# Optimization experiments

Measured on AMD Instinct MI355X. Metric: run time of the kernel, lower is better.

The kernel has to match this reference:

```python
import jax, jax.numpy as jnp
import numpy as np

T = 512   # timesteps (also used as batch-index count for packing)
B = 512   # batch (must equal T for this module's packing to be consistent)
D = 300   # state_dim
H = 128   # hidden_state_dim
E = 64    # embedding_dim
EGO = 12  # ego_state slice fed to the LSTMCell


def setup_inputs() -> dict:
    key = jax.random.key(0)
    ks = jax.random.split(key, 10)
    k = float(1.0 / np.sqrt(H))  # torch LSTMCell uniform init bound
    state = jax.random.normal(ks[0], (T, B, D), dtype=jnp.float32)
    hidden_state = jax.random.normal(ks[1], (B, H), dtype=jnp.float32) * 0.1
    cell_state = jax.random.normal(ks[2], (B, H), dtype=jnp.float32) * 0.1
    len_sequence = jax.random.randint(ks[3], (T,), 1, T + 1, dtype=jnp.int64 if jax.config.jax_enable_x64 else jnp.int32)
    W_ih = jax.random.uniform(ks[4], (4 * H, EGO), minval=-k, maxval=k, dtype=jnp.float32)
    W_hh = jax.random.uniform(ks[5], (4 * H, H), minval=-k, maxval=k, dtype=jnp.float32)
    b_ih = jax.random.uniform(ks[6], (4 * H,), minval=-k, maxval=k, dtype=jnp.float32)
    b_hh = jax.random.uniform(ks[7], (4 * H,), minval=-k, maxval=k, dtype=jnp.float32)
    W_emb = jax.random.normal(ks[8], (E, D + H), dtype=jnp.float32) * 0.05
    b_emb = jnp.zeros((E,), dtype=jnp.float32)
    return dict(state=state, hidden_state=hidden_state, cell_state=cell_state,
                len_sequence=len_sequence, W_ih=W_ih, W_hh=W_hh, b_ih=b_ih,
                b_hh=b_hh, W_emb=W_emb, b_emb=b_emb)


def _pack_indices(L):
    # tmp_output[t][:L[t]] concat over t -> flat indices into [T*B, .] (row-major t,b)
    idx_rnn = np.concatenate([t * B + np.arange(int(L[t])) for t in range(T)]) if T else np.zeros((0,), np.int32)
    # state.permute(1,0,2)[b][:L[b]] concat over b -> flat indices into [B*T, .] (row-major b,t)
    idx_state = np.concatenate([b * T + np.arange(int(L[b])) for b in range(B)]) if B else np.zeros((0,), np.int32)
    return jnp.asarray(idx_rnn, jnp.int32), jnp.asarray(idx_state, jnp.int32)


def _lstm_scan(x_seq, h0, c0, W_ih, W_hh, b_ih, b_hh):
    # torch.nn.LSTMCell math; gate order [i, f, g, o]
    def step(carry, x_t):
        h, c = carry
        gates = x_t @ W_ih.T + b_ih + h @ W_hh.T + b_hh  # [B, 4H]
        i, f, g, o = jnp.split(gates, 4, axis=-1)
        c_new = jax.nn.sigmoid(f) * c + jax.nn.sigmoid(i) * jnp.tanh(g)
        h_new = jax.nn.sigmoid(o) * jnp.tanh(c_new)
        return (h_new, c_new), h_new
    _, hs = jax.lax.scan(step, (h0, c0), x_seq)
    return hs  # [T, B, H]


def reference(state, hidden_state, cell_state, len_sequence, W_ih, W_hh, b_ih, b_hh, W_emb, b_emb):
    L = np.asarray(len_sequence)
    idx_rnn, idx_state = _pack_indices(L)
    rnn_input = state[:, :, :EGO]                               # [T, B, 12]
    hs = _lstm_scan(rnn_input, hidden_state, cell_state, W_ih, W_hh, b_ih, b_hh)  # [T, B, H]
    rnn_packed = hs.reshape(T * B, H)[idx_rnn]                  # [N, H]
    state_packed = jnp.transpose(state, (1, 0, 2)).reshape(B * T, D)[idx_state]  # [N, D]
    feats = jnp.concatenate([state_packed, rnn_packed], axis=1)  # [N, D+H]
    return feats @ W_emb.T + b_emb                               # [N, E]
```

## Files before the change

### kernel.cpp

```cpp
#include <hip/hip_runtime.h>
#include <hip/hip_fp16.h>

#define T_ 512
#define B_ 512
#define D_ 300
#define H_ 128
#define E_ 64
#define EGO_ 12
#define DH_ 428
#define BD_ 153600

typedef __attribute__((ext_vector_type(2))) _Float16 half2_t;
typedef __attribute__((ext_vector_type(8))) _Float16 half8_t;
typedef __attribute__((ext_vector_type(4))) float float4_t;

__device__ __forceinline__ unsigned pack2(float a, float b) {
  __half2 h = __floats2half2_rn(a, b);
  return __builtin_bit_cast(unsigned, h);
}
__device__ __forceinline__ half8_t h8(uint4 u) {
  return __builtin_bit_cast(half8_t, u);
}
__device__ __forceinline__ float sigm(float x) {
  float e = __builtin_amdgcn_exp2f(-1.4426950408889634f * x);
  return __builtin_amdgcn_rcpf(1.0f + e);
}
__device__ __forceinline__ float tanh_(float x) {
  float e = __builtin_amdgcn_exp2f(2.8853900817779268f * x);
  return 1.0f - 2.0f * __builtin_amdgcn_rcpf(1.0f + e);
}

__global__ void prefix_k(const int* __restrict__ L, int* __restrict__ pfx) {
  __shared__ int s[T_];
  int t = threadIdx.x;
  s[t] = L[t];
  __syncthreads();
  for (int off = 1; off < T_; off <<= 1) {
    int v = 0;
    if (t >= off) v = s[t - off];
    __syncthreads();
    s[t] += v;
    __syncthreads();
  }
  if (t == 0) pfx[0] = 0;
  pfx[t + 1] = s[t];
}

#define WS_ 84
#define SST_ 160
__launch_bounds__(256, 1)
__global__ void scan_k(const float* __restrict__ state,
                       const float* __restrict__ h0,
                       const float* __restrict__ c0,
                       const int* __restrict__ lens,
                       const float* __restrict__ W_ih,
                       const float* __restrict__ W_hh,
                       const float* __restrict__ b_ih,
                       const float* __restrict__ b_hh,
                       const float* __restrict__ W_emb,
                       const float* __restrict__ b_emb,
                       const int* __restrict__ pfx,
                       float* __restrict__ out) {
  __shared__ __align__(16) unsigned hb[2][16][WS_];
  __shared__ __align__(16) unsigned sst[2][3][SST_];
  __shared__ int pfx_s[T_], len_s[T_];

  const int tid  = threadIdx.x;
  const int lane = tid & 63;
  const int w    = tid >> 6;
  const int n16  = lane & 15;
  const int quad = lane >> 4;
  const int b0   = blockIdx.x * 2;

  uint4 bfr[4][2][5];
  float bias[4][2];
#pragma unroll
  for (int c = 0; c < 4; ++c) {
#pragma unroll
    for (int p = 0; p < 2; ++p) {
      const int g = c * 128 + w * 32 + 2 * n16 + p;
      bias[c][p] = b_ih[g] + b_hh[g];
#pragma unroll
      for (int s = 0; s < 5; ++s) {
        unsigned pk[4];
#pragma unroll
        for (int pp = 0; pp < 4; ++pp) {
          const int k0 = s * 32 + quad * 8 + 2 * pp;
          float f0 = 0.f, f1 = 0.f;
          if (k0 < 128) { f0 = W_hh[g * H_ + k0]; f1 = W_hh[g * H_ + k0 + 1]; }
          else if (k0 < 140) {
            f0 = W_ih[g * EGO_ + (k0 - 128)];
            if (k0 + 1 < 140) f1 = W_ih[g * EGO_ + (k0 - 127)];
          }
          pk[pp] = pack2(f0, f1);
        }
        bfr[c][p][s] = make_uint4(pk[0], pk[1], pk[2], pk[3]);
      }
    }
  }
  uint4 efr[4], sfr[10];
  const int e_ = w * 16 + n16;
  const float bemb = b_emb[e_];
#pragma unroll
  for (int s = 0; s < 4; ++s) {
    unsigned pk[4];
#pragma unroll
    for (int pp = 0; pp < 4; ++pp) {
      const int k0 = s * 32 + quad * 8 + 2 * pp;
      pk[pp] = pack2(W_emb[e_ * DH_ + D_ + k0], W_emb[e_ * DH_ + D_ + k0 + 1]);
    }
    efr[s] = make_uint4(pk[0], pk[1], pk[2], pk[3]);
  }
#pragma unroll
  for (int s = 0; s < 10; ++s) {
    unsigned pk[4];
#pragma unroll
    for (int pp = 0; pp < 4; ++pp) {
      const int k0 = s * 32 + quad * 8 + 2 * pp;
      float f0 = 0.f, f1 = 0.f;
      if (k0 < D_) { f0 = W_emb[e_ * DH_ + k0]; f1 = W_emb[e_ * DH_ + k0 + 1]; }
      pk[pp] = pack2(f0, f1);
    }
    sfr[s] = make_uint4(pk[0], pk[1], pk[2], pk[3]);
  }

  for (int i = tid; i < 2 * 16 * WS_; i += 256) ((unsigned*)hb)[i] = 0u;
  for (int i = tid; i < 2 * 3 * SST_; i += 256) ((unsigned*)sst)[i] = 0u;
  for (int i = tid; i < T_; i += 256) { pfx_s[i] = pfx[i]; len_s[i] = lens[i]; }
  __syncthreads();
  if (tid < 128) {
    const int r = tid >> 6, d = tid & 63;
    float2 v = ((const float2*)(h0 + (b0 + r) * H_))[d];
    hb[0][4 * r][d] = pack2(v.x, v.y);
  }
  float2 xheld = make_float2(0.f, 0.f);
  if (tid >= 16 && tid < 28) {
    const int j = tid - 16, row = j / 6, jj = j % 6;
    float2 v = ((const float2*)(state + (b0 + row) * D_))[jj];
    hb[0][4 * row][64 + jj] = pack2(v.x, v.y);
    xheld = ((const float2*)(state + BD_ + (b0 + row) * D_))[jj];
  }
  int srow_r = 0, s_i = 0;
  size_t sbase = 0;
  float4 sheld = make_float4(0.f, 0.f, 0.f, 0.f);
  if (tid < 150) {
    srow_r = tid / 75; s_i = tid % 75;
    sbase = (size_t)(b0 + srow_r) * B_ * D_ + 4 * s_i;
    if (b0 + srow_r < len_s[0])
      sheld = *(const float4*)(state + sbase);
  }
  const int rsel = (n16 == 0) ? 0 : ((n16 == 4) ? 1 : 2);
  float cst[2] = {0.f, 0.f};
  if (quad < 2) {
#pragma unroll
    for (int p = 0; p < 2; ++p)
      cst[p] = c0[(b0 + quad) * H_ + w * 32 + 2 * n16 + p];
  }
  __syncthreads();

#pragma unroll 1
  for (int t = 0; t < T_; ++t) {
    const int pb = t & 1;
    float2 xnew = xheld;
    if (tid >= 16 && tid < 28) {
      const int j = tid - 16, row = j / 6, jj = j % 6;
      const int ttx = (t + 2 < T_) ? t + 2 : T_ - 1;
      xnew = ((const float2*)(state + (size_t)ttx * BD_ + (b0 + row) * D_))[jj];
    }
    float4 snew = sheld;
    if (tid < 150) {
      const int tts = (t + 1 < T_) ? t + 1 : T_ - 1;
      if (b0 + srow_r < len_s[tts])
        snew = *(const float4*)(state + sbase + (size_t)tts * D_);
    }

    uint4 a[5];
#pragma unroll
    for (int s = 0; s < 5; ++s)
      a[s] = *(const uint4*)(&hb[pb][n16][s * 16 + quad * 4]);

    if (t > 0) {
      const int Lt = len_s[t - 1];
      if (b0 < Lt) {
        float4_t er  = (float4_t){bemb, bemb, bemb, bemb};
        float4_t es0 = (float4_t){0.f, 0.f, 0.f, 0.f};
        float4_t es1 = (float4_t){0.f, 0.f, 0.f, 0.f};
#pragma unroll
        for (int s = 0; s < 4; ++s)
          er = __builtin_amdgcn_mfma_f32_16x16x32_f16(h8(a[s]), h8(efr[s]), er, 0, 0, 0);
        const unsigned* sb = &sst[pb][rsel][0];
#pragma unroll
        for (int s = 0; s < 5; ++s) {
          uint4 sa = *(const uint4*)(sb + s * 16 + quad * 4);
          es0 = __builtin_amdgcn_mfma_f32_16x16x32_f16(h8(sa), h8(sfr[s]), es0, 0, 0, 0);
        }
#pragma unroll
        for (int s = 5; s < 10; ++s) {
          uint4 sa = *(const uint4*)(sb + s * 16 + quad * 4);
          es1 = __builtin_amdgcn_mfma_f32_16x16x32_f16(h8(sa), h8(sfr[s]), es1, 0, 0, 0);
        }
        if (quad < 2 && b0 + quad < Lt)
          out[((size_t)pfx_s[t - 1] + b0 + quad) * E_ + e_] = er[0] + es0[0] + es1[0];
      }
    }

    float4_t acc[4][2];
#pragma unroll
    for (int c = 0; c < 4; ++c)
#pragma unroll
      for (int p = 0; p < 2; ++p)
        acc[c][p] = (float4_t){bias[c][p], bias[c][p], bias[c][p], bias[c][p]};
#pragma unroll
    for (int s = 0; s < 5; ++s) {
      const half8_t ah = h8(a[s]);
#pragma unroll
      for (int c = 0; c < 4; ++c)
#pragma unroll
        for (int p = 0; p < 2; ++p)
          acc[c][p] = __builtin_amdgcn_mfma_f32_16x16x32_f16(ah, h8(bfr[c][p][s]), acc[c][p], 0, 0, 0);
    }

    if (quad < 2) {
      float hp[2];
#pragma unroll
      for (int p = 0; p < 2; ++p) {
        const float gi = acc[0][p][0];
        const float gf = acc[1][p][0];
        const float gg = acc[2][p][0];
        const float go = acc[3][p][0];
        const float cc = sigm(gf) * cst[p] + sigm(gi) * tanh_(gg);
        cst[p] = cc;
        hp[p] = sigm(go) * tanh_(cc);
      }
      hb[1 - pb][quad * 4][w * 16 + n16] = pack2(hp[0], hp[1]);
    }
    if (tid >= 16 && tid < 28) {
      const int j = tid - 16, row = j / 6, jj = j % 6;
      hb[1 - pb][4 * row][64 + jj] = pack2(xheld.x, xheld.y);
      xheld = xnew;
    }
    if (tid < 150) {
      unsigned* d = &sst[1 - pb][srow_r][2 * s_i];
      d[0] = pack2(sheld.x, sheld.y);
      d[1] = pack2(sheld.z, sheld.w);
      sheld = snew;
    }
    __syncthreads();
  }

  {
    const int Lt = len_s[T_ - 1];
    if (b0 < Lt) {
      float4_t er  = (float4_t){bemb, bemb, bemb, bemb};
      float4_t es0 = (float4_t){0.f, 0.f, 0.f, 0.f};
      float4_t es1 = (float4_t){0.f, 0.f, 0.f, 0.f};
#pragma unroll
      for (int s = 0; s < 4; ++s) {
        uint4 a = *(const uint4*)(&hb[0][n16][s * 16 + quad * 4]);
        er = __builtin_amdgcn_mfma_f32_16x16x32_f16(h8(a), h8(efr[s]), er, 0, 0, 0);
      }
      const unsigned* sb = &sst[0][rsel][0];
#pragma unroll
      for (int s = 0; s < 5; ++s) {
        uint4 sa = *(const uint4*)(sb + s * 16 + quad * 4);
        es0 = __builtin_amdgcn_mfma_f32_16x16x32_f16(h8(sa), h8(sfr[s]), es0, 0, 0, 0);
      }
#pragma unroll
      for (int s = 5; s < 10; ++s) {
        uint4 sa = *(const uint4*)(sb + s * 16 + quad * 4);
        es1 = __builtin_amdgcn_mfma_f32_16x16x32_f16(h8(sa), h8(sfr[s]), es1, 0, 0, 0);
      }
      if (quad < 2 && b0 + quad < Lt)
        out[((size_t)pfx_s[T_ - 1] + b0 + quad) * E_ + e_] = er[0] + es0[0] + es1[0];
    }
  }
}

extern "C" void kernel_launch(void* const* d_in, const int* in_sizes, int n_in,
                              void* d_out, int out_size, void* d_ws, size_t ws_size,
                              hipStream_t stream) {
  const float* state = (const float*)d_in[0];
  const float* h0    = (const float*)d_in[1];
  const float* c0    = (const float*)d_in[2];
  const int*   lens  = (const int*)d_in[3];
  const float* W_ih  = (const float*)d_in[4];
  const float* W_hh  = (const float*)d_in[5];
  const float* b_ih  = (const float*)d_in[6];
  const float* b_hh  = (const float*)d_in[7];
  const float* W_emb = (const float*)d_in[8];
  const float* b_emb = (const float*)d_in[9];
  float* out = (float*)d_out;
  int* pfx = (int*)d_ws;

  prefix_k<<<1, T_, 0, stream>>>(lens, pfx);
  scan_k<<<B_ / 2, 256, 0, stream>>>(state, h0, c0, lens, W_ih, W_hh, b_ih, b_hh,
                                     W_emb, b_emb, pfx, out);
}
```

Measured before the change: 941.6 us.

## Batch embedding projection over four timesteps into full MFMA tiles

The per-step embedding matmul used only two of the sixteen MFMA rows and ran every timestep. Now h and state rows are buffered into double-buffered 16-row staging tiles across four timesteps, and one batched embedding MFMA pass runs every fourth step. State prefetch moves two steps ahead to fill these tiles. The goal is fewer embedding MFMAs on the serial LSTM critical path, at the cost of extra shared memory and a burstier step every fourth iteration.

Result: faster. 859.1 us (-8.8%).

```diff
diff --git a/kernel.cpp b/kernel.cpp
--- a/kernel.cpp
+++ b/kernel.cpp
@@ -47,7 +47,8 @@
 }
 
 #define WS_ 84
-#define SST_ 160
+#define HH_ 84
+#define SST_ 164
 __launch_bounds__(256, 1)
 __global__ void scan_k(const float* __restrict__ state,
                        const float* __restrict__ h0,
@@ -62,7 +63,8 @@
                        const int* __restrict__ pfx,
                        float* __restrict__ out) {
   __shared__ __align__(16) unsigned hb[2][16][WS_];
-  __shared__ __align__(16) unsigned sst[2][3][SST_];
+  __shared__ __align__(16) unsigned hh[2][16][HH_];
+  __shared__ __align__(16) unsigned sst[2][16][SST_];
   __shared__ int pfx_s[T_], len_s[T_];
 
   const int tid  = threadIdx.x;
@@ -125,7 +127,8 @@
   }
 
   for (int i = tid; i < 2 * 16 * WS_; i += 256) ((unsigned*)hb)[i] = 0u;
-  for (int i = tid; i < 2 * 3 * SST_; i += 256) ((unsigned*)sst)[i] = 0u;
+  for (int i = tid; i < 2 * 16 * HH_; i += 256) ((unsigned*)hh)[i] = 0u;
+  for (int i = tid; i < 2 * 16 * SST_; i += 256) ((unsigned*)sst)[i] = 0u;
   for (int i = tid; i < T_; i += 256) { pfx_s[i] = pfx[i]; len_s[i] = lens[i]; }
   __syncthreads();
   if (tid < 128) {
@@ -142,14 +145,14 @@
   }
   int srow_r = 0, s_i = 0;
   size_t sbase = 0;
-  float4 sheld = make_float4(0.f, 0.f, 0.f, 0.f);
+  float4 sheld0 = make_float4(0.f, 0.f, 0.f, 0.f);
+  float4 sheld1 = make_float4(0.f, 0.f, 0.f, 0.f);
   if (tid < 150) {
     srow_r = tid / 75; s_i = tid % 75;
     sbase = (size_t)(b0 + srow_r) * B_ * D_ + 4 * s_i;
-    if (b0 + srow_r < len_s[0])
-      sheld = *(const float4*)(state + sbase);
-  }
-  const int rsel = (n16 == 0) ? 0 : ((n16 == 4) ? 1 : 2);
+    if (b0 + srow_r < len_s[0]) sheld0 = *(const float4*)(state + sbase);
+    if (b0 + srow_r < len_s[1]) sheld1 = *(const float4*)(state + sbase + D_);
+  }
   float cst[2] = {0.f, 0.f};
   if (quad < 2) {
 #pragma unroll
@@ -161,15 +164,16 @@
 #pragma unroll 1
   for (int t = 0; t < T_; ++t) {
     const int pb = t & 1;
+    const int gp = (t >> 2) & 1;
     float2 xnew = xheld;
     if (tid >= 16 && tid < 28) {
       const int j = tid - 16, row = j / 6, jj = j % 6;
       const int ttx = (t + 2 < T_) ? t + 2 : T_ - 1;
       xnew = ((const float2*)(state + (size_t)ttx * BD_ + (b0 + row) * D_))[jj];
     }
-    float4 snew = sheld;
+    float4 snew = make_float4(0.f, 0.f, 0.f, 0.f);
     if (tid < 150) {
-      const int tts = (t + 1 < T_) ? t + 1 : T_ - 1;
+      const int tts = (t + 2 < T_) ? t + 2 : T_ - 1;
       if (b0 + srow_r < len_s[tts])
         snew = *(const float4*)(state + sbase + (size_t)tts * D_);
     }
@@ -179,28 +183,35 @@
     for (int s = 0; s < 5; ++s)
       a[s] = *(const uint4*)(&hb[pb][n16][s * 16 + quad * 4]);
 
-    if (t > 0) {
-      const int Lt = len_s[t - 1];
-      if (b0 < Lt) {
-        float4_t er  = (float4_t){bemb, bemb, bemb, bemb};
-        float4_t es0 = (float4_t){0.f, 0.f, 0.f, 0.f};
-        float4_t es1 = (float4_t){0.f, 0.f, 0.f, 0.f};
-#pragma unroll
-        for (int s = 0; s < 4; ++s)
-          er = __builtin_amdgcn_mfma_f32_16x16x32_f16(h8(a[s]), h8(efr[s]), er, 0, 0, 0);
-        const unsigned* sb = &sst[pb][rsel][0];
-#pragma unroll
-        for (int s = 0; s < 5; ++s) {
-          uint4 sa = *(const uint4*)(sb + s * 16 + quad * 4);
-          es0 = __builtin_amdgcn_mfma_f32_16x16x32_f16(h8(sa), h8(sfr[s]), es0, 0, 0, 0);
+    if ((t & 3) == 0 && t > 0) {
+      const int rb = 1 - gp;
+      float4_t er  = (float4_t){bemb, bemb, bemb, bemb};
+      float4_t es0 = (float4_t){0.f, 0.f, 0.f, 0.f};
+      float4_t es1 = (float4_t){0.f, 0.f, 0.f, 0.f};
+#pragma unroll
+      for (int s = 0; s < 4; ++s) {
+        uint4 ha = *(const uint4*)(&hh[rb][n16][s * 16 + quad * 4]);
+        er = __builtin_amdgcn_mfma_f32_16x16x32_f16(h8(ha), h8(efr[s]), er, 0, 0, 0);
+      }
+#pragma unroll
+      for (int s = 0; s < 5; ++s) {
+        uint4 sa = *(const uint4*)(&sst[rb][n16][s * 16 + quad * 4]);
+        es0 = __builtin_amdgcn_mfma_f32_16x16x32_f16(h8(sa), h8(sfr[s]), es0, 0, 0, 0);
+      }
+#pragma unroll
+      for (int s = 5; s < 10; ++s) {
+        uint4 sa = *(const uint4*)(&sst[rb][n16][s * 16 + quad * 4]);
+        es1 = __builtin_amdgcn_mfma_f32_16x16x32_f16(h8(sa), h8(sfr[s]), es1, 0, 0, 0);
+      }
+      if (quad < 2) {
+#pragma unroll
+        for (int r = 0; r < 4; ++r) {
+          const int R  = quad * 4 + r;
+          const int seg = (t - 4) + (R >> 1);
+          const int br  = R & 1;
+          if (b0 + br < len_s[seg])
+            out[((size_t)pfx_s[seg] + b0 + br) * E_ + e_] = er[r] + es0[r] + es1[r];
         }
-#pragma unroll
-        for (int s = 5; s < 10; ++s) {
-          uint4 sa = *(const uint4*)(sb + s * 16 + quad * 4);
-          es1 = __builtin_amdgcn_mfma_f32_16x16x32_f16(h8(sa), h8(sfr[s]), es1, 0, 0, 0);
-        }
-        if (quad < 2 && b0 + quad < Lt)
-          out[((size_t)pfx_s[t - 1] + b0 + quad) * E_ + e_] = er[0] + es0[0] + es1[0];
       }
     }
 
@@ -232,7 +243,9 @@
         cst[p] = cc;
         hp[p] = sigm(go) * tanh_(cc);
       }
-      hb[1 - pb][quad * 4][w * 16 + n16] = pack2(hp[0], hp[1]);
+      const unsigned hpk = pack2(hp[0], hp[1]);
+      hb[1 - pb][quad * 4][w * 16 + n16] = hpk;
+      hh[gp][2 * (t & 3) + quad][w * 16 + n16] = hpk;
     }
     if (tid >= 16 && tid < 28) {
       const int j = tid - 16, row = j / 6, jj = j % 6;
@@ -240,38 +253,44 @@
       xheld = xnew;
     }
     if (tid < 150) {
-      unsigned* d = &sst[1 - pb][srow_r][2 * s_i];
-      d[0] = pack2(sheld.x, sheld.y);
-      d[1] = pack2(sheld.z, sheld.w);
-      sheld = snew;
+      unsigned* d = &sst[gp][2 * (t & 3) + srow_r][2 * s_i];
+      d[0] = pack2(sheld0.x, sheld0.y);
+      d[1] = pack2(sheld0.z, sheld0.w);
+      sheld0 = sheld1;
+      sheld1 = snew;
     }
     __syncthreads();
   }
 
   {
-    const int Lt = len_s[T_ - 1];
-    if (b0 < Lt) {
-      float4_t er  = (float4_t){bemb, bemb, bemb, bemb};
-      float4_t es0 = (float4_t){0.f, 0.f, 0.f, 0.f};
-      float4_t es1 = (float4_t){0.f, 0.f, 0.f, 0.f};
-#pragma unroll
-      for (int s = 0; s < 4; ++s) {
-        uint4 a = *(const uint4*)(&hb[0][n16][s * 16 + quad * 4]);
-        er = __builtin_amdgcn_mfma_f32_16x16x32_f16(h8(a), h8(efr[s]), er, 0, 0, 0);
-      }
-      const unsigned* sb = &sst[0][rsel][0];
-#pragma unroll
-      for (int s = 0; s < 5; ++s) {
-        uint4 sa = *(const uint4*)(sb + s * 16 + quad * 4);
-        es0 = __builtin_amdgcn_mfma_f32_16x16x32_f16(h8(sa), h8(sfr[s]), es0, 0, 0, 0);
-      }
-#pragma unroll
-      for (int s = 5; s < 10; ++s) {
-        uint4 sa = *(const uint4*)(sb + s * 16 + quad * 4);
-        es1 = __builtin_amdgcn_mfma_f32_16x16x32_f16(h8(sa), h8(sfr[s]), es1, 0, 0, 0);
-      }
-      if (quad < 2 && b0 + quad < Lt)
-        out[((size_t)pfx_s[T_ - 1] + b0 + quad) * E_ + e_] = er[0] + es0[0] + es1[0];
+    const int rb = 1 - ((T_ >> 2) & 1);
+    float4_t er  = (float4_t){bemb, bemb, bemb, bemb};
+    float4_t es0 = (float4_t){0.f, 0.f, 0.f, 0.f};
+    float4_t es1 = (float4_t){0.f, 0.f, 0.f, 0.f};
+#pragma unroll
+    for (int s = 0; s < 4; ++s) {
+      uint4 ha = *(const uint4*)(&hh[rb][n16][s * 16 + quad * 4]);
+      er = __builtin_amdgcn_mfma_f32_16x16x32_f16(h8(ha), h8(efr[s]), er, 0, 0, 0);
+    }
+#pragma unroll
+    for (int s = 0; s < 5; ++s) {
+      uint4 sa = *(const uint4*)(&sst[rb][n16][s * 16 + quad * 4]);
+      es0 = __builtin_amdgcn_mfma_f32_16x16x32_f16(h8(sa), h8(sfr[s]), es0, 0, 0, 0);
+    }
+#pragma unroll
+    for (int s = 5; s < 10; ++s) {
+      uint4 sa = *(const uint4*)(&sst[rb][n16][s * 16 + quad * 4]);
+      es1 = __builtin_amdgcn_mfma_f32_16x16x32_f16(h8(sa), h8(sfr[s]), es1, 0, 0, 0);
+    }
+    if (quad < 2) {
+#pragma unroll
+      for (int r = 0; r < 4; ++r) {
+        const int R  = quad * 4 + r;
+        const int seg = (T_ - 4) + (R >> 1);
+        const int br  = R & 1;
+        if (b0 + br < len_s[seg])
+          out[((size_t)pfx_s[seg] + b0 + br) * E_ + e_] = er[r] + es0[r] + es1[r];
+      }
     }
   }
 }
```
